# Performance work log

Hardware: AMD Instinct MI355X
Metric: run time of the kernel (lower is better)

Reference implementation:

```python
import jax, jax.numpy as jnp
import numpy as np

N_NODES = 20000
N_EDGES = 160000
N_GRAPHS = 64
X_DIM = 9
E_DIM = 1
U_RAW = 4096
U_DIM = 256
E_HID = 1024
E_OUT = 512
N_HID = 512
N_OUT = 1


def _lin_params(k, fan_in, fan_out):
    kw, kb = jax.random.split(k)
    bound = 1.0 / np.sqrt(fan_in)
    W = jax.random.uniform(kw, (fan_in, fan_out), jnp.float32, -bound, bound)
    b = jax.random.uniform(kb, (fan_out,), jnp.float32, -bound, bound)
    return W, b


def setup_inputs() -> dict:
    key = jax.random.key(0)
    ks = jax.random.split(key, 16)
    x = jax.random.normal(ks[0], (N_NODES, X_DIM), jnp.float32)
    edge_attr = jax.random.normal(ks[1], (N_EDGES, E_DIM), jnp.float32)
    u = jax.random.normal(ks[2], (N_GRAPHS, U_RAW), jnp.float32)
    edge_index = jax.random.randint(ks[3], (2, N_EDGES), 0, N_NODES, jnp.int64)
    batch = jax.random.randint(ks[4], (N_NODES,), 0, N_GRAPHS, jnp.int64)

    Wsel, bsel = _lin_params(ks[5], U_RAW, U_DIM)
    e_in = E_DIM + 2 * X_DIM + U_DIM  # 275
    eW1, eb1 = _lin_params(ks[6], e_in, E_HID)
    eW2, eb2 = _lin_params(ks[7], E_HID, E_HID)
    eW3, eb3 = _lin_params(ks[8], E_HID, E_HID)
    eW4, eb4 = _lin_params(ks[9], E_HID, E_HID)
    eW5, eb5 = _lin_params(ks[10], E_HID, E_OUT)
    n1W1, n1b1 = _lin_params(ks[11], E_OUT + X_DIM, N_HID)  # 521
    n1W2, n1b2 = _lin_params(ks[12], N_HID, N_HID)
    n2W1, n2b1 = _lin_params(ks[13], X_DIM + N_HID + U_DIM, N_HID)  # 777
    n2W2, n2b2 = _lin_params(ks[14], N_HID, N_OUT)

    return dict(x=x, edge_attr=edge_attr, u=u, edge_index=edge_index, batch=batch,
                Wsel=Wsel, bsel=bsel,
                eW1=eW1, eb1=eb1, eW2=eW2, eb2=eb2, eW3=eW3, eb3=eb3,
                eW4=eW4, eb4=eb4, eW5=eW5, eb5=eb5,
                n1W1=n1W1, n1b1=n1b1, n1W2=n1W2, n1b2=n1b2,
                n2W1=n2W1, n2b1=n2b1, n2W2=n2W2, n2b2=n2b2)


def _forward(x, edge_attr, u, edge_index, batch,
             Wsel, bsel, eW1, eb1, eW2, eb2, eW3, eb3, eW4, eb4, eW5, eb5,
             n1W1, n1b1, n1W2, n1b2, n2W1, n2b1, n2W2, n2b2):
    relu = jax.nn.relu
    u2 = u @ Wsel + bsel  # [B, 256]
    row, col = edge_index[0], edge_index[1]

    # EdgeModel: cat([src, dest, edge_attr, u[batch[row]]]) -> 5-layer MLP
    e = jnp.concatenate([x[row], x[col], edge_attr, u2[batch[row]]], axis=1)
    e = relu(e @ eW1 + eb1)
    e = relu(e @ eW2 + eb2)
    e = relu(e @ eW3 + eb3)
    e = relu(e @ eW4 + eb4)
    e = e @ eW5 + eb5  # [E, 512]

    # NodeModel: gather x[col], MLP1, scatter_mean over row, MLP2
    h = jnp.concatenate([x[col], e], axis=1)
    h = relu(h @ n1W1 + n1b1)
    h = relu(h @ n1W2 + n1b2)  # [E, 512]
    ssum = jax.ops.segment_sum(h, row, num_segments=x.shape[0])
    cnt = jax.ops.segment_sum(jnp.ones((h.shape[0],), h.dtype), row, num_segments=x.shape[0])
    agg = ssum / jnp.maximum(cnt, 1.0)[:, None]  # scatter_mean

    z = jnp.concatenate([x, agg, u2[batch]], axis=1)
    z = relu(z @ n2W1 + n2b1)
    z = z @ n2W2 + n2b2  # [N, 1]
    return jnp.squeeze(z)


def reference(x, edge_attr, u, edge_index, batch,
              Wsel, bsel, eW1, eb1, eW2, eb2, eW3, eb3, eW4, eb4, eW5, eb5,
              n1W1, n1b1, n1W2, n1b2, n2W1, n2b1, n2W2, n2b2):
    return _forward(x, edge_attr, u, edge_index, batch,
                    Wsel, bsel, eW1, eb1, eW2, eb2, eW3, eb3, eW4, eb4, eW5, eb5,
                    n1W1, n1b1, n1W2, n1b2, n2W1, n2b1, n2W2, n2b2)
```

## Files before the change

### kernel.cpp

```cpp
#include <hip/hip_runtime.h>

typedef _Float16 f16;
typedef __attribute__((ext_vector_type(8))) _Float16 f16x8;
typedef __attribute__((ext_vector_type(4))) float f32x4;

#define E_TOTAL 160000
#define NN 20000
#define NGRAPH 64

__device__ __forceinline__ void gl_lds16(const void* g, void* l) {
    __builtin_amdgcn_global_load_lds((const __attribute__((address_space(1))) void*)g,
                                     (__attribute__((address_space(3))) void*)l, 16, 0, 0);
}

#define MFMA16(a, b, c) __builtin_amdgcn_mfma_f32_16x16x32_f16((a), (b), (c), 0, 0, 0)
#define LGKM(n) do { asm volatile("s_waitcnt lgkmcnt(" #n ")" ::: "memory"); \
                     __builtin_amdgcn_sched_barrier(0); } while (0)
#define VMW4  asm volatile("s_waitcnt vmcnt(4)" ::: "memory")
#define VMW0  asm volatile("s_waitcnt vmcnt(0)" ::: "memory")
#define SBAR  __builtin_amdgcn_s_barrier()
#define SCHED0 __builtin_amdgcn_sched_barrier(0)

template <int RELU, int AUXU, int AUXX, int SCAT>
__global__ __launch_bounds__(512, 2) void hgemm8(
    int M, int N, int K,
    const f16* __restrict__ A, int lda,
    const f16* __restrict__ Bt,
    f16* __restrict__ C, int ldc,
    const float* __restrict__ bias,
    const f16* __restrict__ utab, const int* __restrict__ uidx,
    const float* __restrict__ x9, const int* __restrict__ xidx, const float* __restrict__ W9,
    float* __restrict__ sout, const int* __restrict__ sidx)
{
    __shared__ __align__(16) char Ash[2][2][16384];
    __shared__ __align__(16) char Bsh[2][2][16384];
    __shared__ float Ws9[AUXX ? 2304 : 1];

    const int tid  = threadIdx.x;
    const int lane = tid & 63;
    const int w    = tid >> 6;

    const int nbn = gridDim.x;
    const int nwg = nbn * gridDim.y;
    int d  = blockIdx.y * nbn + blockIdx.x;
    int q8 = nwg >> 3, r8 = nwg & 7;
    int xk = d & 7, j8 = d >> 3;
    int wl = (xk < r8 ? xk * (q8 + 1) : r8 * (q8 + 1) + (xk - r8) * q8) + j8;
    const int bm = (wl / nbn) * 256;
    const int bn = (wl % nbn) * 256;

    const int wm = (w >> 2) * 128;
    const int wn = (w & 3) * 64;
    const int fr = lane & 15;
    const int kq = lane >> 4;

    const char* Ab = (const char*)A;
    const char* Bb = (const char*)Bt;
    const size_t lda2 = (size_t)lda * 2;
    const size_t ldb2 = (size_t)K * 2;

    f32x4 acc[8][4] = {};

    int aoff[8], boff[4];
#pragma unroll
    for (int mi = 0; mi < 8; ++mi) {
        int r = wm + mi * 16 + fr;
        aoff[mi] = r * 64 + ((kq ^ ((r >> 1) & 3)) << 4);
    }
#pragma unroll
    for (int ni = 0; ni < 4; ++ni) {
        int r = wn + ni * 16 + fr;
        boff[ni] = r * 64 + ((kq ^ ((r >> 1) & 3)) << 4);
    }

    int sdest[2];
    size_t gsrcA[2], gsrcB[2];
#pragma unroll
    for (int i = 0; i < 2; ++i) {
        int L = i * 8192 + tid * 16;
        int row = L >> 6;
        int s = (L >> 4) & 3;
        int sw = (s ^ ((row >> 1) & 3)) << 4;
        sdest[i] = L;
        gsrcA[i] = (size_t)(bm + row) * lda2 + sw;
        gsrcB[i] = (size_t)(bn + row) * ldb2 + sw;
    }

    const int NT = K >> 6;

    auto stageA = [&](int t, int h, int buf) {
        size_t kb = (size_t)t * 128 + h * 64;
#pragma unroll
        for (int i = 0; i < 2; ++i)
            gl_lds16(Ab + gsrcA[i] + kb, &Ash[buf][h][0] + sdest[i]);
    };
    auto stageB = [&](int t, int h, int buf) {
        size_t kb = (size_t)t * 128 + h * 64;
#pragma unroll
        for (int i = 0; i < 2; ++i)
            gl_lds16(Bb + gsrcB[i] + kb, &Bsh[buf][h][0] + sdest[i]);
    };

    f16x8 a0[4], b0[4], a1[4], a2[4], b2[4], a3[4];

    stageA(0, 0, 0); stageB(0, 0, 0); stageA(0, 1, 0); stageB(0, 1, 0);
    VMW4;
    SBAR;
#pragma unroll
    for (int i = 0; i < 4; ++i) a0[i] = *(const f16x8*)(&Ash[0][0][0] + aoff[i]);
#pragma unroll
    for (int i = 0; i < 4; ++i) b0[i] = *(const f16x8*)(&Bsh[0][0][0] + boff[i]);

    for (int t = 0; t < NT; ++t) {
        const int cur = t & 1, nxt = cur ^ 1;
        const bool pre = (t + 1 < NT);
        const char* A0 = &Ash[cur][0][0];
        const char* A1 = &Ash[cur][1][0];
        const char* B1 = &Bsh[cur][1][0];

#pragma unroll
        for (int i = 0; i < 4; ++i) a1[i] = *(const f16x8*)(A0 + aoff[4 + i]);
        if (pre) stageA(t + 1, 0, nxt);
        SBAR;
        LGKM(4);
        __builtin_amdgcn_s_setprio(1);
#pragma unroll
        for (int mi = 0; mi < 4; ++mi)
#pragma unroll
            for (int ni = 0; ni < 4; ++ni)
                acc[mi][ni] = MFMA16(a0[mi], b0[ni], acc[mi][ni]);
        __builtin_amdgcn_s_setprio(0);
        SBAR;

        if (pre) stageB(t + 1, 0, nxt);
        SBAR;
        LGKM(0);
        if (pre) { VMW4; } else { VMW0; }
        SBAR;
#pragma unroll
        for (int i = 0; i < 4; ++i) a2[i] = *(const f16x8*)(A1 + aoff[i]);
#pragma unroll
        for (int i = 0; i < 4; ++i) b2[i] = *(const f16x8*)(B1 + boff[i]);
        SCHED0;
        __builtin_amdgcn_s_setprio(1);
#pragma unroll
        for (int mi = 0; mi < 4; ++mi)
#pragma unroll
            for (int ni = 0; ni < 4; ++ni)
                acc[4 + mi][ni] = MFMA16(a1[mi], b0[ni], acc[4 + mi][ni]);
        __builtin_amdgcn_s_setprio(0);
        SBAR;

#pragma unroll
        for (int i = 0; i < 4; ++i) a3[i] = *(const f16x8*)(A1 + aoff[4 + i]);
        if (pre) stageA(t + 1, 1, nxt);
        SBAR;
        LGKM(4);
        __builtin_amdgcn_s_setprio(1);
#pragma unroll
        for (int mi = 0; mi < 4; ++mi)
#pragma unroll
            for (int ni = 0; ni < 4; ++ni)
                acc[mi][ni] = MFMA16(a2[mi], b2[ni], acc[mi][ni]);
        __builtin_amdgcn_s_setprio(0);
        SBAR;

        if (pre) stageB(t + 1, 1, nxt);
        SBAR;
        LGKM(0);
        if (pre) {
            VMW4;
            SBAR;
            const char* An = &Ash[nxt][0][0];
            const char* Bn = &Bsh[nxt][0][0];
#pragma unroll
            for (int i = 0; i < 4; ++i) a0[i] = *(const f16x8*)(An + aoff[i]);
#pragma unroll
            for (int i = 0; i < 4; ++i) b0[i] = *(const f16x8*)(Bn + boff[i]);
            SCHED0;
        }
        __builtin_amdgcn_s_setprio(1);
#pragma unroll
        for (int mi = 0; mi < 4; ++mi)
#pragma unroll
            for (int ni = 0; ni < 4; ++ni)
                acc[4 + mi][ni] = MFMA16(a3[mi], b2[ni], acc[4 + mi][ni]);
        __builtin_amdgcn_s_setprio(0);
        SBAR;
    }

    if (AUXX) {
        for (int i = tid; i < 9 * 256; i += 512)
            Ws9[i] = W9[(size_t)(i >> 8) * N + bn + (i & 255)];
        __syncthreads();
    }

#pragma unroll
    for (int mi = 0; mi < 8; ++mi) {
        int r0 = bm + wm + mi * 16 + kq * 4;
#pragma unroll
        for (int r = 0; r < 4; ++r) {
            int grow = r0 + r;
            if (grow >= M) continue;
            int ub = 0;
            if (AUXU) ub = uidx[grow];
            int sb = 0;
            if (SCAT) sb = sidx[grow];
            float xv[9];
            if (AUXX) {
                int xi = xidx ? xidx[grow] : grow;
#pragma unroll
                for (int q = 0; q < 9; ++q) xv[q] = x9[(size_t)xi * 9 + q];
            }
#pragma unroll
            for (int ni = 0; ni < 4; ++ni) {
                int lcol = wn + ni * 16 + fr;
                int col = bn + lcol;
                float v = acc[mi][ni][r] + bias[col];
                if (AUXU) v += (float)utab[(size_t)ub * N + col];
                if (AUXX) {
                    float s = 0.f;
#pragma unroll
                    for (int q = 0; q < 9; ++q) s = fmaf(xv[q], Ws9[q * 256 + lcol], s);
                    v += s;
                }
                if (RELU) v = fmaxf(v, 0.f);
                if (SCAT) {
                    atomicAdd(sout + (size_t)sb * N + col, v);
                } else {
                    C[(size_t)grow * ldc + col] = (f16)v;
                }
            }
        }
    }
}

struct WtJob { const float* src; f16* dst; int r0, ks, n, kp, tr; };
struct WtJobs { WtJob j[10]; };

__global__ void k_wtall(WtJobs js)
{
    WtJob jb = js.j[blockIdx.y];
    size_t tot = (size_t)jb.n * jb.kp;
    size_t t = (size_t)blockIdx.x * 256 + threadIdx.x;
    if (t >= tot) return;
    if (jb.tr) {
        int n = (int)(t / jb.kp), k = (int)(t % jb.kp);
        jb.dst[t] = (k < jb.ks) ? (f16)jb.src[(size_t)(jb.r0 + k) * jb.n + n] : (f16)0.f;
    } else {
        jb.dst[t] = (f16)jb.src[t];
    }
}

__global__ void k_cbias(const float* __restrict__ n1W1, const float* __restrict__ eb5,
                        const float* __restrict__ n1b1, float* __restrict__ cb)
{
    int b = blockIdx.x * 256 + threadIdx.x;
    if (b >= 512) return;
    float s = n1b1[b];
    for (int c = 0; c < 512; ++c) s = fmaf(eb5[c], n1W1[(size_t)(9 + c) * 512 + b], s);
    cb[b] = s;
}

__global__ __launch_bounds__(256) void k_u2b(const float* __restrict__ u,
                                             const float* __restrict__ Wsel,
                                             const float* __restrict__ bsel,
                                             f16* __restrict__ u2h)
{
    __shared__ float us[4096];
    __shared__ float red[256];
    const int g = blockIdx.y;
    const int c0 = blockIdx.x * 16;
    const int col = threadIdx.x & 15;
    const int kp = threadIdx.x >> 4;
    for (int i = threadIdx.x; i < 4096; i += 256) us[i] = u[(size_t)g * 4096 + i];
    __syncthreads();
    float acc = 0.f;
    const float* wp = Wsel + (size_t)(kp * 256) * 256 + c0 + col;
#pragma unroll 8
    for (int i = 0; i < 256; ++i) acc = fmaf(us[kp * 256 + i], wp[(size_t)i * 256], acc);
    red[threadIdx.x] = acc;
    __syncthreads();
    if (kp < 8) red[threadIdx.x] += red[threadIdx.x + 128];
    __syncthreads();
    if (kp < 4) red[threadIdx.x] += red[threadIdx.x + 64];
    __syncthreads();
    if (kp < 2) red[threadIdx.x] += red[threadIdx.x + 32];
    __syncthreads();
    if (kp == 0)
        u2h[(size_t)g * 256 + c0 + col] = (f16)(red[threadIdx.x] + red[threadIdx.x + 16] + bsel[c0 + col]);
}

__global__ void k_gather19(const float* __restrict__ x, const float* __restrict__ eattr,
                           const int* __restrict__ ei, const int* __restrict__ batch,
                           f16* __restrict__ feat, int* __restrict__ ebat)
{
    size_t t = (size_t)blockIdx.x * 256 + threadIdx.x;
    if (t >= (size_t)E_TOTAL * 64) return;
    int i = (int)(t >> 6), j = (int)(t & 63);
    float v = 0.f;
    if (j < 9)        v = x[ei[i] * 9 + j];
    else if (j < 18)  v = x[ei[E_TOTAL + i] * 9 + (j - 9)];
    else if (j == 18) v = eattr[i];
    else if (j == 19) ebat[i] = batch[ei[i]];
    feat[t] = (f16)v;
}

__global__ void k_cnt(const int* __restrict__ ei, float* __restrict__ cnt)
{
    int t = blockIdx.x * 256 + threadIdx.x;
    if (t < E_TOTAL) atomicAdd(cnt + ei[t], 1.0f);
}

__global__ void k_agg(const float* __restrict__ ssum, const float* __restrict__ cnt,
                      f16* __restrict__ agg)
{
    size_t t = (size_t)blockIdx.x * 256 + threadIdx.x;
    if (t >= (size_t)NN * 512) return;
    int n = (int)(t >> 9);
    agg[t] = (f16)(ssum[t] / fmaxf(cnt[n], 1.f));
}

__global__ void k_final(const f16* __restrict__ z1, const float* __restrict__ W,
                        const float* __restrict__ b, float* __restrict__ out)
{
    int gt = blockIdx.x * 256 + threadIdx.x;
    int row = gt >> 6;
    int lane = threadIdx.x & 63;
    if (row >= NN) return;
    float s = 0.f;
#pragma unroll
    for (int c = lane; c < 512; c += 64) s += (float)z1[(size_t)row * 512 + c] * W[c];
#pragma unroll
    for (int off = 32; off; off >>= 1) s += __shfl_down(s, off);
    if (lane == 0) out[row] = s + b[0];
}


extern "C" void kernel_launch(void* const* d_in, const int* in_sizes, int n_in,
                              void* d_out, int out_size, void* d_ws, size_t ws_size,
                              hipStream_t stream)
{
    const float* x     = (const float*)d_in[0];
    const float* eattr = (const float*)d_in[1];
    const float* u     = (const float*)d_in[2];
    const int*   ei    = (const int*)d_in[3];
    const int*   batch = (const int*)d_in[4];
    const float* Wsel  = (const float*)d_in[5];
    const float* bsel  = (const float*)d_in[6];
    const float* eW1 = (const float*)d_in[7],  * eb1 = (const float*)d_in[8];
    const float* eW2 = (const float*)d_in[9],  * eb2 = (const float*)d_in[10];
    const float* eW3 = (const float*)d_in[11], * eb3 = (const float*)d_in[12];
    const float* eW4 = (const float*)d_in[13], * eb4 = (const float*)d_in[14];
    const float* eW5 = (const float*)d_in[15], * eb5 = (const float*)d_in[16];
    const float* n1W1 = (const float*)d_in[17], * n1b1 = (const float*)d_in[18];
    const float* n1W2 = (const float*)d_in[19], * n1b2 = (const float*)d_in[20];
    const float* n2W1 = (const float*)d_in[21], * n2b1 = (const float*)d_in[22];
    const float* n2W2 = (const float*)d_in[23], * n2b2 = (const float*)d_in[24];
    float* out = (float*)d_out;

    char* ws = (char*)d_ws;
    size_t off = 0;
    auto alc = [&](size_t bytes) { char* p = ws + off; off += (bytes + 255) & ~(size_t)255; return p; };

    float* ssum  = (float*)alc((size_t)NN * 512 * 4);
    float* cnt   = (float*)alc((size_t)NN * 4);
    float* zbias = (float*)alc(1024 * 4);
    float* cbias = (float*)alc(512 * 4);
    f16* u2h     = (f16*)alc((size_t)256 * 256 * 2);
    f16* ubias_e = (f16*)alc((size_t)64 * 1024 * 2);
    f16* ubias_n = (f16*)alc((size_t)64 * 512 * 2);
    f16* eW1t19  = (f16*)alc((size_t)1024 * 64 * 2);
    f16* eW1ut   = (f16*)alc((size_t)1024 * 256 * 2);
    f16* eW2t    = (f16*)alc((size_t)1024 * 1024 * 2);
    f16* eW3t    = (f16*)alc((size_t)1024 * 1024 * 2);
    f16* eW4t    = (f16*)alc((size_t)1024 * 1024 * 2);
    f16* eW5h    = (f16*)alc((size_t)1024 * 512 * 2);
    f16* combo_t = (f16*)alc((size_t)512 * 1024 * 2);
    f16* n1W1et  = (f16*)alc((size_t)512 * 512 * 2);
    f16* n1W2t   = (f16*)alc((size_t)512 * 512 * 2);
    f16* n2W1et  = (f16*)alc((size_t)512 * 512 * 2);
    f16* n2W1ut  = (f16*)alc((size_t)512 * 256 * 2);
    f16* featAll = (f16*)alc((size_t)E_TOTAL * 64 * 2);
    int* ebatAll = (int*)alc((size_t)E_TOTAL * 4);
    size_t fixed = off;

    size_t per_edge = 4096;
    size_t need_ro = (size_t)20224 * 512 * 2 * 2;
    size_t avail = ws_size > fixed ? ws_size - fixed : 0;
    long long Cmax = (long long)(avail / per_edge);
    int C;
    if (Cmax >= E_TOTAL)      C = E_TOTAL;
    else if (Cmax >= 16384)   C = (int)((Cmax / 16384) * 16384);
    else                      C = (int)((Cmax / 256) * 256);
    if ((size_t)C * per_edge < need_ro)
        C = (int)(((need_ro + per_edge - 1) / per_edge + 255) / 256 * 256);

    f16* buf1 = (f16*)(ws + fixed);
    f16* buf2 = buf1 + (size_t)C * 1024;
    f16* agg  = (f16*)(ws + fixed);
    f16* z1   = agg + (size_t)20224 * 512;

    size_t zlen = (size_t)((char*)cbias - (char*)ssum) + 512 * 4;
    hipMemsetAsync(ssum, 0, zlen, stream);

    WtJobs js;
    js.j[0] = {eW1,  eW1t19, 0,   19,   1024, 64,   1};
    js.j[1] = {eW1,  eW1ut,  19,  256,  1024, 256,  1};
    js.j[2] = {eW2,  eW2t,   0,   1024, 1024, 1024, 1};
    js.j[3] = {eW3,  eW3t,   0,   1024, 1024, 1024, 1};
    js.j[4] = {eW4,  eW4t,   0,   1024, 1024, 1024, 1};
    js.j[5] = {n1W1, n1W1et, 9,   512,  512,  512,  1};
    js.j[6] = {n1W2, n1W2t,  0,   512,  512,  512,  1};
    js.j[7] = {n2W1, n2W1et, 9,   512,  512,  512,  1};
    js.j[8] = {n2W1, n2W1ut, 521, 256,  512,  256,  1};
    js.j[9] = {eW5,  eW5h,   0,   0,    1024, 512,  0};
    k_wtall<<<dim3(4096, 10), 256, 0, stream>>>(js);

    k_u2b<<<dim3(16, NGRAPH), 256, 0, stream>>>(u, Wsel, bsel, u2h);
    k_cnt<<<(E_TOTAL + 255) / 256, 256, 0, stream>>>(ei, cnt);
    k_cbias<<<2, 256, 0, stream>>>(n1W1, eb5, n1b1, cbias);
    k_gather19<<<(unsigned)(((size_t)E_TOTAL * 64 + 255) / 256), 256, 0, stream>>>(
        x, eattr, ei, batch, featAll, ebatAll);

    hgemm8<0,0,0,0><<<dim3(4, 1), 512, 0, stream>>>(64, 1024, 256, u2h, 256, eW1ut,
        ubias_e, 1024, eb1, nullptr, nullptr, nullptr, nullptr, nullptr, nullptr, nullptr);
    hgemm8<0,0,0,0><<<dim3(2, 1), 512, 0, stream>>>(64, 512, 256, u2h, 256, n2W1ut,
        ubias_n, 512, n2b1, nullptr, nullptr, nullptr, nullptr, nullptr, nullptr, nullptr);

    hgemm8<0,0,0,0><<<dim3(4, 2), 512, 0, stream>>>(512, 1024, 512, n1W1et, 512, eW5h,
        combo_t, 1024, zbias, nullptr, nullptr, nullptr, nullptr, nullptr, nullptr, nullptr);

    for (int e0 = 0; e0 < E_TOTAL; e0 += C) {
        int Ce = E_TOTAL - e0 < C ? E_TOTAL - e0 : C;
        int gy = (Ce + 255) / 256;

        hgemm8<1,1,0,0><<<dim3(4, gy), 512, 0, stream>>>(Ce, 1024, 64,
            featAll + (size_t)e0 * 64, 64, eW1t19,
            buf1, 1024, zbias, ubias_e, ebatAll + e0, nullptr, nullptr, nullptr, nullptr, nullptr);
        hgemm8<1,0,0,0><<<dim3(4, gy), 512, 0, stream>>>(Ce, 1024, 1024, buf1, 1024, eW2t,
            buf2, 1024, eb2, nullptr, nullptr, nullptr, nullptr, nullptr, nullptr, nullptr);
        hgemm8<1,0,0,0><<<dim3(4, gy), 512, 0, stream>>>(Ce, 1024, 1024, buf2, 1024, eW3t,
            buf1, 1024, eb3, nullptr, nullptr, nullptr, nullptr, nullptr, nullptr, nullptr);
        hgemm8<1,0,0,0><<<dim3(4, gy), 512, 0, stream>>>(Ce, 1024, 1024, buf1, 1024, eW4t,
            buf2, 1024, eb4, nullptr, nullptr, nullptr, nullptr, nullptr, nullptr, nullptr);

        hgemm8<1,0,1,0><<<dim3(2, gy), 512, 0, stream>>>(Ce, 512, 1024, buf2, 1024, combo_t,
            buf1, 512, cbias, nullptr, nullptr, x, ei + E_TOTAL + e0, n1W1, nullptr, nullptr);

        hgemm8<1,0,0,1><<<dim3(2, gy), 512, 0, stream>>>(Ce, 512, 512, buf1, 512, n1W2t,
            nullptr, 512, n1b2, nullptr, nullptr, nullptr, nullptr, nullptr, ssum, ei + e0);
    }

    k_agg<<<(unsigned)(((size_t)NN * 512 + 255) / 256), 256, 0, stream>>>(ssum, cnt, agg);
    hgemm8<1,1,1,0><<<dim3(2, 79), 512, 0, stream>>>(NN, 512, 512, agg, 512, n2W1et,
        z1, 512, zbias, ubias_n, batch, x, nullptr, n2W1, nullptr, nullptr);
    k_final<<<(NN * 64 + 255) / 256, 256, 0, stream>>>(z1, n2W2, n2b2, out);
}
```

Baseline: 2.213 ms.

## Add 256x512-tile triple-buffered GEMM for the three 1024x1024 edge layers

```diff
diff --git a/kernel.cpp b/kernel.cpp
--- a/kernel.cpp
+++ b/kernel.cpp
@@ -16,10 +16,124 @@
 #define MFMA16(a, b, c) __builtin_amdgcn_mfma_f32_16x16x32_f16((a), (b), (c), 0, 0, 0)
 #define LGKM(n) do { asm volatile("s_waitcnt lgkmcnt(" #n ")" ::: "memory"); \
                      __builtin_amdgcn_sched_barrier(0); } while (0)
+#define VMW6  asm volatile("s_waitcnt vmcnt(6)" ::: "memory")
 #define VMW4  asm volatile("s_waitcnt vmcnt(4)" ::: "memory")
 #define VMW0  asm volatile("s_waitcnt vmcnt(0)" ::: "memory")
 #define SBAR  __builtin_amdgcn_s_barrier()
 #define SCHED0 __builtin_amdgcn_sched_barrier(0)
+
+__global__ __launch_bounds__(512) void hgemmW(
+    int M, int N, int K,
+    const f16* __restrict__ A, int lda,
+    const f16* __restrict__ Bt,
+    f16* __restrict__ C, int ldc,
+    const float* __restrict__ bias)
+{
+    __shared__ __align__(16) char L[3][49152];
+    const int tid  = threadIdx.x;
+    const int lane = tid & 63;
+    const int w    = tid >> 6;
+
+    const int nbn = gridDim.x;
+    const int nwg = nbn * gridDim.y;
+    int d  = blockIdx.y * nbn + blockIdx.x;
+    int q8 = nwg >> 3, r8 = nwg & 7;
+    int xk = d & 7, j8 = d >> 3;
+    int wl = (xk < r8 ? xk * (q8 + 1) : r8 * (q8 + 1) + (xk - r8) * q8) + j8;
+    const int bm = (wl / nbn) * 256;
+    const int bn = (wl % nbn) * 512;
+
+    const int wm = (w >> 2) * 128;
+    const int wn = (w & 3) * 128;
+    const int fr = lane & 15;
+    const int kq = lane >> 4;
+
+    const char* Ab = (const char*)A;
+    const char* Bb = (const char*)Bt;
+    const size_t lda2 = (size_t)lda * 2;
+    const size_t ldb2 = (size_t)K * 2;
+
+    f32x4 acc[8][8] = {};
+
+    int aoff[8], boff[8];
+#pragma unroll
+    for (int mi = 0; mi < 8; ++mi) {
+        int r = wm + mi * 16 + fr;
+        aoff[mi] = r * 64 + ((kq ^ ((r >> 1) & 3)) << 4);
+    }
+#pragma unroll
+    for (int ni = 0; ni < 8; ++ni) {
+        int r = wn + ni * 16 + fr;
+        boff[ni] = 16384 + r * 64 + ((kq ^ ((r >> 1) & 3)) << 4);
+    }
+
+    int sdest[6];
+    size_t gsrcA[2], gsrcB[4];
+#pragma unroll
+    for (int i = 0; i < 6; ++i) {
+        int Lo = i * 8192 + tid * 16;
+        int row = Lo >> 6;
+        int slot = (Lo >> 4) & 3;
+        int sw = (slot ^ ((row >> 1) & 3)) << 4;
+        sdest[i] = Lo;
+        if (i < 2) gsrcA[i] = (size_t)(bm + row) * lda2 + sw;
+        else       gsrcB[i - 2] = (size_t)(bn + row - 256) * ldb2 + sw;
+    }
+
+    auto stage = [&](int t, int buf) {
+        size_t kb = (size_t)t * 64;
+#pragma unroll
+        for (int i = 0; i < 2; ++i) gl_lds16(Ab + gsrcA[i] + kb, &L[buf][0] + sdest[i]);
+#pragma unroll
+        for (int i = 0; i < 4; ++i) gl_lds16(Bb + gsrcB[i] + kb, &L[buf][0] + sdest[2 + i]);
+    };
+
+    const int NT = K >> 5;
+    stage(0, 0);
+    stage(1, 1);
+
+    int buf = 0;
+    for (int t = 0; t < NT; ++t) {
+        if (t + 1 < NT) { VMW6; } else { VMW0; }
+        SBAR;
+        const char* base = &L[buf][0];
+        f16x8 a[8], b[8];
+#pragma unroll
+        for (int i = 0; i < 8; ++i) a[i] = *(const f16x8*)(base + aoff[i]);
+#pragma unroll
+        for (int i = 0; i < 8; ++i) b[i] = *(const f16x8*)(base + boff[i]);
+        int nb = buf + 2; if (nb >= 3) nb -= 3;
+        if (t + 2 < NT) stage(t + 2, nb);
+        LGKM(0);
+        __builtin_amdgcn_s_setprio(1);
+#pragma unroll
+        for (int mi = 0; mi < 8; ++mi)
+#pragma unroll
+            for (int ni = 0; ni < 8; ++ni)
+                acc[mi][ni] = MFMA16(a[mi], b[ni], acc[mi][ni]);
+        __builtin_amdgcn_s_setprio(0);
+        ++buf; if (buf == 3) buf = 0;
+    }
+
+    float bz[8];
+#pragma unroll
+    for (int ni = 0; ni < 8; ++ni) bz[ni] = bias[bn + wn + ni * 16 + fr];
+#pragma unroll
+    for (int mi = 0; mi < 8; ++mi) {
+        int r0 = bm + wm + mi * 16 + kq * 4;
+#pragma unroll
+        for (int r = 0; r < 4; ++r) {
+            int grow = r0 + r;
+            if (grow >= M) continue;
+#pragma unroll
+            for (int ni = 0; ni < 8; ++ni) {
+                int col = bn + wn + ni * 16 + fr;
+                float v = fmaxf(acc[mi][ni][r] + bz[ni], 0.f);
+                C[(size_t)grow * ldc + col] = (f16)v;
+            }
+        }
+    }
+}
 
 template <int RELU, int AUXU, int AUXX, int SCAT>
 __global__ __launch_bounds__(512, 2) void hgemm8(
@@ -77,11 +191,11 @@
     size_t gsrcA[2], gsrcB[2];
 #pragma unroll
     for (int i = 0; i < 2; ++i) {
-        int L = i * 8192 + tid * 16;
-        int row = L >> 6;
-        int s = (L >> 4) & 3;
+        int Lo = i * 8192 + tid * 16;
+        int row = Lo >> 6;
+        int s = (Lo >> 4) & 3;
         int sw = (s ^ ((row >> 1) & 3)) << 4;
-        sdest[i] = L;
+        sdest[i] = Lo;
         gsrcA[i] = (size_t)(bm + row) * lda2 + sw;
         gsrcB[i] = (size_t)(bn + row) * ldb2 + sw;
     }
@@ -438,12 +552,10 @@
         hgemm8<1,1,0,0><<<dim3(4, gy), 512, 0, stream>>>(Ce, 1024, 64,
             featAll + (size_t)e0 * 64, 64, eW1t19,
             buf1, 1024, zbias, ubias_e, ebatAll + e0, nullptr, nullptr, nullptr, nullptr, nullptr);
-        hgemm8<1,0,0,0><<<dim3(4, gy), 512, 0, stream>>>(Ce, 1024, 1024, buf1, 1024, eW2t,
-            buf2, 1024, eb2, nullptr, nullptr, nullptr, nullptr, nullptr, nullptr, nullptr);
-        hgemm8<1,0,0,0><<<dim3(4, gy), 512, 0, stream>>>(Ce, 1024, 1024, buf2, 1024, eW3t,
-            buf1, 1024, eb3, nullptr, nullptr, nullptr, nullptr, nullptr, nullptr, nullptr);
-        hgemm8<1,0,0,0><<<dim3(4, gy), 512, 0, stream>>>(Ce, 1024, 1024, buf1, 1024, eW4t,
-            buf2, 1024, eb4, nullptr, nullptr, nullptr, nullptr, nullptr, nullptr, nullptr);
+
+        hgemmW<<<dim3(2, gy), 512, 0, stream>>>(Ce, 1024, 1024, buf1, 1024, eW2t, buf2, 1024, eb2);
+        hgemmW<<<dim3(2, gy), 512, 0, stream>>>(Ce, 1024, 1024, buf2, 1024, eW3t, buf1, 1024, eb3);
+        hgemmW<<<dim3(2, gy), 512, 0, stream>>>(Ce, 1024, 1024, buf1, 1024, eW4t, buf2, 1024, eb4);
 
         hgemm8<1,0,1,0><<<dim3(2, gy), 512, 0, stream>>>(Ce, 512, 1024, buf2, 1024, combo_t,
             buf1, 512, cbias, nullptr, nullptr, x, ei + E_TOTAL + e0, n1W1, nullptr, nullptr);
```

Measured after the change: 8.306 ms. 275% more time.

## Load B operand straight from global into registers, bypassing LDS

Applied to the files above, without the earlier changes.

```diff
diff --git a/kernel.cpp b/kernel.cpp
--- a/kernel.cpp
+++ b/kernel.cpp
@@ -16,13 +16,15 @@
 #define MFMA16(a, b, c) __builtin_amdgcn_mfma_f32_16x16x32_f16((a), (b), (c), 0, 0, 0)
 #define LGKM(n) do { asm volatile("s_waitcnt lgkmcnt(" #n ")" ::: "memory"); \
                      __builtin_amdgcn_sched_barrier(0); } while (0)
-#define VMW4  asm volatile("s_waitcnt vmcnt(4)" ::: "memory")
+#define VMW12 asm volatile("s_waitcnt vmcnt(12)" ::: "memory")
 #define VMW0  asm volatile("s_waitcnt vmcnt(0)" ::: "memory")
 #define SBAR  __builtin_amdgcn_s_barrier()
 #define SCHED0 __builtin_amdgcn_sched_barrier(0)
 
+struct BF { f16x8 v[4][2]; };
+
 template <int RELU, int AUXU, int AUXX, int SCAT>
-__global__ __launch_bounds__(512, 2) void hgemm8(
+__global__ __launch_bounds__(512, 2) void hgemmB(
     int M, int N, int K,
     const f16* __restrict__ A, int lda,
     const f16* __restrict__ Bt,
@@ -33,7 +35,6 @@
     float* __restrict__ sout, const int* __restrict__ sidx)
 {
     __shared__ __align__(16) char Ash[2][2][16384];
-    __shared__ __align__(16) char Bsh[2][2][16384];
     __shared__ float Ws9[AUXX ? 2304 : 1];
 
     const int tid  = threadIdx.x;
@@ -61,133 +62,89 @@
 
     f32x4 acc[8][4] = {};
 
-    int aoff[8], boff[4];
+    int aoff[8];
 #pragma unroll
     for (int mi = 0; mi < 8; ++mi) {
         int r = wm + mi * 16 + fr;
         aoff[mi] = r * 64 + ((kq ^ ((r >> 1) & 3)) << 4);
     }
-#pragma unroll
-    for (int ni = 0; ni < 4; ++ni) {
-        int r = wn + ni * 16 + fr;
-        boff[ni] = r * 64 + ((kq ^ ((r >> 1) & 3)) << 4);
-    }
 
     int sdest[2];
-    size_t gsrcA[2], gsrcB[2];
+    size_t gsrcA[2];
 #pragma unroll
     for (int i = 0; i < 2; ++i) {
-        int L = i * 8192 + tid * 16;
-        int row = L >> 6;
-        int s = (L >> 4) & 3;
+        int Lo = i * 8192 + tid * 16;
+        int row = Lo >> 6;
+        int s = (Lo >> 4) & 3;
         int sw = (s ^ ((row >> 1) & 3)) << 4;
-        sdest[i] = L;
+        sdest[i] = Lo;
         gsrcA[i] = (size_t)(bm + row) * lda2 + sw;
-        gsrcB[i] = (size_t)(bn + row) * ldb2 + sw;
-    }
+    }
+
+    const char* bbase[4];
+#pragma unroll
+    for (int ni = 0; ni < 4; ++ni)
+        bbase[ni] = Bb + (size_t)(bn + wn + ni * 16 + fr) * ldb2 + kq * 16;
 
     const int NT = K >> 6;
 
-    auto stageA = [&](int t, int h, int buf) {
-        size_t kb = (size_t)t * 128 + h * 64;
-#pragma unroll
-        for (int i = 0; i < 2; ++i)
-            gl_lds16(Ab + gsrcA[i] + kb, &Ash[buf][h][0] + sdest[i]);
+    auto stageA = [&](int t, int buf) {
+        size_t kb = (size_t)t << 7;
+#pragma unroll
+        for (int h = 0; h < 2; ++h)
+#pragma unroll
+            for (int i = 0; i < 2; ++i)
+                gl_lds16(Ab + gsrcA[i] + kb + h * 64, &Ash[buf][h][0] + sdest[i]);
     };
-    auto stageB = [&](int t, int h, int buf) {
-        size_t kb = (size_t)t * 128 + h * 64;
-#pragma unroll
-        for (int i = 0; i < 2; ++i)
-            gl_lds16(Bb + gsrcB[i] + kb, &Bsh[buf][h][0] + sdest[i]);
+    auto loadB = [&](BF& dst, int t) {
+        size_t kb = (size_t)t << 7;
+#pragma unroll
+        for (int ni = 0; ni < 4; ++ni)
+#pragma unroll
+            for (int ks = 0; ks < 2; ++ks)
+                dst.v[ni][ks] = *(const f16x8*)(bbase[ni] + kb + ks * 64);
     };
-
-    f16x8 a0[4], b0[4], a1[4], a2[4], b2[4], a3[4];
-
-    stageA(0, 0, 0); stageB(0, 0, 0); stageA(0, 1, 0); stageB(0, 1, 0);
-    VMW4;
-    SBAR;
-#pragma unroll
-    for (int i = 0; i < 4; ++i) a0[i] = *(const f16x8*)(&Ash[0][0][0] + aoff[i]);
-#pragma unroll
-    for (int i = 0; i < 4; ++i) b0[i] = *(const f16x8*)(&Bsh[0][0][0] + boff[i]);
-
-    for (int t = 0; t < NT; ++t) {
-        const int cur = t & 1, nxt = cur ^ 1;
+    auto body = [&](int t, int buf, const BF& cur, BF& nxt) {
         const bool pre = (t + 1 < NT);
-        const char* A0 = &Ash[cur][0][0];
-        const char* A1 = &Ash[cur][1][0];
-        const char* B1 = &Bsh[cur][1][0];
-
-#pragma unroll
-        for (int i = 0; i < 4; ++i) a1[i] = *(const f16x8*)(A0 + aoff[4 + i]);
-        if (pre) stageA(t + 1, 0, nxt);
+        if (pre) {
+            stageA(t + 1, buf ^ 1);
+            loadB(nxt, t + 1);
+            SCHED0;
+            VMW12;
+        } else {
+            VMW0;
+        }
         SBAR;
-        LGKM(4);
-        __builtin_amdgcn_s_setprio(1);
-#pragma unroll
-        for (int mi = 0; mi < 4; ++mi)
-#pragma unroll
-            for (int ni = 0; ni < 4; ++ni)
-                acc[mi][ni] = MFMA16(a0[mi], b0[ni], acc[mi][ni]);
-        __builtin_amdgcn_s_setprio(0);
+#pragma unroll
+        for (int ks = 0; ks < 2; ++ks) {
+            const char* half = &Ash[buf][ks][0];
+#pragma unroll
+            for (int g = 0; g < 2; ++g) {
+                f16x8 a[4];
+#pragma unroll
+                for (int i = 0; i < 4; ++i) a[i] = *(const f16x8*)(half + aoff[g * 4 + i]);
+                LGKM(0);
+                __builtin_amdgcn_s_setprio(1);
+#pragma unroll
+                for (int mi = 0; mi < 4; ++mi)
+#pragma unroll
+                    for (int ni = 0; ni < 4; ++ni)
+                        acc[g * 4 + mi][ni] = MFMA16(a[mi], cur.v[ni][ks], acc[g * 4 + mi][ni]);
+                __builtin_amdgcn_s_setprio(0);
+            }
+        }
         SBAR;
-
-        if (pre) stageB(t + 1, 0, nxt);
-        SBAR;
-        LGKM(0);
-        if (pre) { VMW4; } else { VMW0; }
-        SBAR;
-#pragma unroll
-        for (int i = 0; i < 4; ++i) a2[i] = *(const f16x8*)(A1 + aoff[i]);
-#pragma unroll
-        for (int i = 0; i < 4; ++i) b2[i] = *(const f16x8*)(B1 + boff[i]);
-        SCHED0;
-        __builtin_amdgcn_s_setprio(1);
-#pragma unroll
-        for (int mi = 0; mi < 4; ++mi)
-#pragma unroll
-            for (int ni = 0; ni < 4; ++ni)
-                acc[4 + mi][ni] = MFMA16(a1[mi], b0[ni], acc[4 + mi][ni]);
-        __builtin_amdgcn_s_setprio(0);
-        SBAR;
-
-#pragma unroll
-        for (int i = 0; i < 4; ++i) a3[i] = *(const f16x8*)(A1 + aoff[4 + i]);
-        if (pre) stageA(t + 1, 1, nxt);
-        SBAR;
-        LGKM(4);
-        __builtin_amdgcn_s_setprio(1);
-#pragma unroll
-        for (int mi = 0; mi < 4; ++mi)
-#pragma unroll
-            for (int ni = 0; ni < 4; ++ni)
-                acc[mi][ni] = MFMA16(a2[mi], b2[ni], acc[mi][ni]);
-        __builtin_amdgcn_s_setprio(0);
-        SBAR;
-
-        if (pre) stageB(t + 1, 1, nxt);
-        SBAR;
-        LGKM(0);
-        if (pre) {
-            VMW4;
-            SBAR;
-            const char* An = &Ash[nxt][0][0];
-            const char* Bn = &Bsh[nxt][0][0];
-#pragma unroll
-            for (int i = 0; i < 4; ++i) a0[i] = *(const f16x8*)(An + aoff[i]);
-#pragma unroll
-            for (int i = 0; i < 4; ++i) b0[i] = *(const f16x8*)(Bn + boff[i]);
-            SCHED0;
-        }
-        __builtin_amdgcn_s_setprio(1);
-#pragma unroll
-        for (int mi = 0; mi < 4; ++mi)
-#pragma unroll
-            for (int ni = 0; ni < 4; ++ni)
-                acc[4 + mi][ni] = MFMA16(a3[mi], b2[ni], acc[4 + mi][ni]);
-        __builtin_amdgcn_s_setprio(0);
-        SBAR;
-    }
+    };
+
+    BF bf0, bf1;
+    stageA(0, 0);
+    loadB(bf0, 0);
+    int t = 0;
+    for (; t + 2 <= NT; t += 2) {
+        body(t,     0, bf0, bf1);
+        body(t + 1, 1, bf1, bf0);
+    }
+    if (t < NT) body(t, t & 1, bf0, bf1);
 
     if (AUXX) {
         for (int i = tid; i < 9 * 256; i += 512)
@@ -423,37 +380,37 @@
     k_gather19<<<(unsigned)(((size_t)E_TOTAL * 64 + 255) / 256), 256, 0, stream>>>(
         x, eattr, ei, batch, featAll, ebatAll);
 
-    hgemm8<0,0,0,0><<<dim3(4, 1), 512, 0, stream>>>(64, 1024, 256, u2h, 256, eW1ut,
+    hgemmB<0,0,0,0><<<dim3(4, 1), 512, 0, stream>>>(64, 1024, 256, u2h, 256, eW1ut,
         ubias_e, 1024, eb1, nullptr, nullptr, nullptr, nullptr, nullptr, nullptr, nullptr);
-    hgemm8<0,0,0,0><<<dim3(2, 1), 512, 0, stream>>>(64, 512, 256, u2h, 256, n2W1ut,
+    hgemmB<0,0,0,0><<<dim3(2, 1), 512, 0, stream>>>(64, 512, 256, u2h, 256, n2W1ut,
         ubias_n, 512, n2b1, nullptr, nullptr, nullptr, nullptr, nullptr, nullptr, nullptr);
 
-    hgemm8<0,0,0,0><<<dim3(4, 2), 512, 0, stream>>>(512, 1024, 512, n1W1et, 512, eW5h,
+    hgemmB<0,0,0,0><<<dim3(4, 2), 512, 0, stream>>>(512, 1024, 512, n1W1et, 512, eW5h,
         combo_t, 1024, zbias, nullptr, nullptr, nullptr, nullptr, nullptr, nullptr, nullptr);
 
     for (int e0 = 0; e0 < E_TOTAL; e0 += C) {
         int Ce = E_TOTAL - e0 < C ? E_TOTAL - e0 : C;
         int gy = (Ce + 255) / 256;
 
-        hgemm8<1,1,0,0><<<dim3(4, gy), 512, 0, stream>>>(Ce, 1024, 64,
+        hgemmB<1,1,0,0><<<dim3(4, gy), 512, 0, stream>>>(Ce, 1024, 64,
             featAll + (size_t)e0 * 64, 64, eW1t19,
             buf1, 1024, zbias, ubias_e, ebatAll + e0, nullptr, nullptr, nullptr, nullptr, nullptr);
-        hgemm8<1,0,0,0><<<dim3(4, gy), 512, 0, stream>>>(Ce, 1024, 1024, buf1, 1024, eW2t,
+        hgemmB<1,0,0,0><<<dim3(4, gy), 512, 0, stream>>>(Ce, 1024, 1024, buf1, 1024, eW2t,
             buf2, 1024, eb2, nullptr, nullptr, nullptr, nullptr, nullptr, nullptr, nullptr);
-        hgemm8<1,0,0,0><<<dim3(4, gy), 512, 0, stream>>>(Ce, 1024, 1024, buf2, 1024, eW3t,
+        hgemmB<1,0,0,0><<<dim3(4, gy), 512, 0, stream>>>(Ce, 1024, 1024, buf2, 1024, eW3t,
             buf1, 1024, eb3, nullptr, nullptr, nullptr, nullptr, nullptr, nullptr, nullptr);
-        hgemm8<1,0,0,0><<<dim3(4, gy), 512, 0, stream>>>(Ce, 1024, 1024, buf1, 1024, eW4t,
+        hgemmB<1,0,0,0><<<dim3(4, gy), 512, 0, stream>>>(Ce, 1024, 1024, buf1, 1024, eW4t,
             buf2, 1024, eb4, nullptr, nullptr, nullptr, nullptr, nullptr, nullptr, nullptr);
 
-        hgemm8<1,0,1,0><<<dim3(2, gy), 512, 0, stream>>>(Ce, 512, 1024, buf2, 1024, combo_t,
+        hgemmB<1,0,1,0><<<dim3(2, gy), 512, 0, stream>>>(Ce, 512, 1024, buf2, 1024, combo_t,
             buf1, 512, cbias, nullptr, nullptr, x, ei + E_TOTAL + e0, n1W1, nullptr, nullptr);
 
-        hgemm8<1,0,0,1><<<dim3(2, gy), 512, 0, stream>>>(Ce, 512, 512, buf1, 512, n1W2t,
+        hgemmB<1,0,0,1><<<dim3(2, gy), 512, 0, stream>>>(Ce, 512, 512, buf1, 512, n1W2t,
             nullptr, 512, n1b2, nullptr, nullptr, nullptr, nullptr, nullptr, ssum, ei + e0);
     }
 
     k_agg<<<(unsigned)(((size_t)NN * 512 + 255) / 256), 256, 0, stream>>>(ssum, cnt, agg);
-    hgemm8<1,1,1,0><<<dim3(2, 79), 512, 0, stream>>>(NN, 512, 512, agg, 512, n2W1et,
+    hgemmB<1,1,1,0><<<dim3(2, 79), 512, 0, stream>>>(NN, 512, 512, agg, 512, n2W1et,
         z1, 512, zbias, ubias_n, batch, x, nullptr, n2W1, nullptr, nullptr);
     k_final<<<(NN * 64 + 255) / 256, 256, 0, stream>>>(z1, n2W2, n2b2, out);
 }
```

Measured after the change: 4.088 ms. 84.7% more time.

## Sort edges by source node and replace atomic scatter with segmented reduction

Applied to the files above, without the earlier changes.

```diff
diff --git a/kernel.cpp b/kernel.cpp
--- a/kernel.cpp
+++ b/kernel.cpp
@@ -21,7 +21,7 @@
 #define SBAR  __builtin_amdgcn_s_barrier()
 #define SCHED0 __builtin_amdgcn_sched_barrier(0)
 
-template <int RELU, int AUXU, int AUXX, int SCAT>
+template <int RELU, int AUXU, int AUXX>
 __global__ __launch_bounds__(512, 2) void hgemm8(
     int M, int N, int K,
     const f16* __restrict__ A, int lda,
@@ -29,8 +29,7 @@
     f16* __restrict__ C, int ldc,
     const float* __restrict__ bias,
     const f16* __restrict__ utab, const int* __restrict__ uidx,
-    const float* __restrict__ x9, const int* __restrict__ xidx, const float* __restrict__ W9,
-    float* __restrict__ sout, const int* __restrict__ sidx)
+    const float* __restrict__ x9, const int* __restrict__ xidx, const float* __restrict__ W9)
 {
     __shared__ __align__(16) char Ash[2][2][16384];
     __shared__ __align__(16) char Bsh[2][2][16384];
@@ -77,11 +76,11 @@
     size_t gsrcA[2], gsrcB[2];
 #pragma unroll
     for (int i = 0; i < 2; ++i) {
-        int L = i * 8192 + tid * 16;
-        int row = L >> 6;
-        int s = (L >> 4) & 3;
+        int Lo = i * 8192 + tid * 16;
+        int row = Lo >> 6;
+        int s = (Lo >> 4) & 3;
         int sw = (s ^ ((row >> 1) & 3)) << 4;
-        sdest[i] = L;
+        sdest[i] = Lo;
         gsrcA[i] = (size_t)(bm + row) * lda2 + sw;
         gsrcB[i] = (size_t)(bn + row) * ldb2 + sw;
     }
@@ -204,8 +203,6 @@
             if (grow >= M) continue;
             int ub = 0;
             if (AUXU) ub = uidx[grow];
-            int sb = 0;
-            if (SCAT) sb = sidx[grow];
             float xv[9];
             if (AUXX) {
                 int xi = xidx ? xidx[grow] : grow;
@@ -225,11 +222,7 @@
                     v += s;
                 }
                 if (RELU) v = fmaxf(v, 0.f);
-                if (SCAT) {
-                    atomicAdd(sout + (size_t)sb * N + col, v);
-                } else {
-                    C[(size_t)grow * ldc + col] = (f16)v;
-                }
+                C[(size_t)grow * ldc + col] = (f16)v;
             }
         }
     }
@@ -291,25 +284,86 @@
         u2h[(size_t)g * 256 + c0 + col] = (f16)(red[threadIdx.x] + red[threadIdx.x + 16] + bsel[c0 + col]);
 }
 
+__global__ void k_cnt(const int* __restrict__ ei, float* __restrict__ cnt)
+{
+    int t = blockIdx.x * 256 + threadIdx.x;
+    if (t < E_TOTAL) atomicAdd(cnt + ei[t], 1.0f);
+}
+
+__global__ __launch_bounds__(256) void k_scan(const float* __restrict__ cnt,
+                                              int* __restrict__ offs, int* __restrict__ cursor)
+{
+    __shared__ int part[256];
+    const int tid = threadIdx.x;
+    const int n0 = tid * 79;
+    int s = 0;
+    for (int i = 0; i < 79; ++i) {
+        int n = n0 + i;
+        if (n < NN) s += (int)cnt[n];
+    }
+    part[tid] = s;
+    __syncthreads();
+    for (int dstep = 1; dstep < 256; dstep <<= 1) {
+        int add = (tid >= dstep) ? part[tid - dstep] : 0;
+        __syncthreads();
+        part[tid] += add;
+        __syncthreads();
+    }
+    int run = part[tid] - s;
+    for (int i = 0; i < 79; ++i) {
+        int n = n0 + i;
+        if (n < NN) {
+            offs[n] = run;
+            cursor[n] = run;
+            run += (int)cnt[n];
+        }
+    }
+    if (tid == 255) offs[NN] = E_TOTAL;
+}
+
+__global__ void k_perm(const int* __restrict__ ei, int* __restrict__ cursor,
+                       int* __restrict__ perm)
+{
+    int e = blockIdx.x * 256 + threadIdx.x;
+    if (e < E_TOTAL) {
+        int pos = atomicAdd(cursor + ei[e], 1);
+        perm[pos] = e;
+    }
+}
+
 __global__ void k_gather19(const float* __restrict__ x, const float* __restrict__ eattr,
                            const int* __restrict__ ei, const int* __restrict__ batch,
-                           f16* __restrict__ feat, int* __restrict__ ebat)
+                           const int* __restrict__ perm,
+                           f16* __restrict__ feat, int* __restrict__ ebat, int* __restrict__ colA)
 {
     size_t t = (size_t)blockIdx.x * 256 + threadIdx.x;
     if (t >= (size_t)E_TOTAL * 64) return;
-    int i = (int)(t >> 6), j = (int)(t & 63);
+    int j = (int)(t >> 6), jj = (int)(t & 63);
+    int e = perm[j];
     float v = 0.f;
-    if (j < 9)        v = x[ei[i] * 9 + j];
-    else if (j < 18)  v = x[ei[E_TOTAL + i] * 9 + (j - 9)];
-    else if (j == 18) v = eattr[i];
-    else if (j == 19) ebat[i] = batch[ei[i]];
+    if (jj < 9)        v = x[ei[e] * 9 + jj];
+    else if (jj < 18)  v = x[ei[E_TOTAL + e] * 9 + (jj - 9)];
+    else if (jj == 18) v = eattr[e];
+    else if (jj == 19) ebat[j] = batch[ei[e]];
+    else if (jj == 20) colA[j] = ei[E_TOTAL + e];
     feat[t] = (f16)v;
 }
 
-__global__ void k_cnt(const int* __restrict__ ei, float* __restrict__ cnt)
-{
-    int t = blockIdx.x * 256 + threadIdx.x;
-    if (t < E_TOTAL) atomicAdd(cnt + ei[t], 1.0f);
+__global__ void k_seg(int e0, int Ce, const f16* __restrict__ h2,
+                      const int* __restrict__ offs, float* __restrict__ ssum)
+{
+    size_t t = (size_t)blockIdx.x * 256 + threadIdx.x;
+    if (t >= (size_t)NN * 512) return;
+    int n = (int)(t >> 9), col = (int)(t & 511);
+    int lo = offs[n], hi = offs[n + 1];
+    int e1 = e0 + Ce;
+    if (lo < e0) lo = e0;
+    if (hi > e1) hi = e1;
+    if (lo >= hi) return;
+    float s = 0.f;
+    for (int j = lo; j < hi; ++j)
+        s += (float)h2[(size_t)(j - e0) * 512 + col];
+    ssum[t] += s;
 }
 
 __global__ void k_agg(const float* __restrict__ ssum, const float* __restrict__ cnt,
@@ -381,8 +435,12 @@
     f16* n1W2t   = (f16*)alc((size_t)512 * 512 * 2);
     f16* n2W1et  = (f16*)alc((size_t)512 * 512 * 2);
     f16* n2W1ut  = (f16*)alc((size_t)512 * 256 * 2);
+    int* offs    = (int*)alc((size_t)(NN + 1) * 4);
+    int* cursor  = (int*)alc((size_t)NN * 4);
+    int* perm    = (int*)alc((size_t)E_TOTAL * 4);
     f16* featAll = (f16*)alc((size_t)E_TOTAL * 64 * 2);
     int* ebatAll = (int*)alc((size_t)E_TOTAL * 4);
+    int* colAll  = (int*)alc((size_t)E_TOTAL * 4);
     size_t fixed = off;
 
     size_t per_edge = 4096;
@@ -419,41 +477,46 @@
 
     k_u2b<<<dim3(16, NGRAPH), 256, 0, stream>>>(u, Wsel, bsel, u2h);
     k_cnt<<<(E_TOTAL + 255) / 256, 256, 0, stream>>>(ei, cnt);
+    k_scan<<<1, 256, 0, stream>>>(cnt, offs, cursor);
+    k_perm<<<(E_TOTAL + 255) / 256, 256, 0, stream>>>(ei, cursor, perm);
     k_cbias<<<2, 256, 0, stream>>>(n1W1, eb5, n1b1, cbias);
     k_gather19<<<(unsigned)(((size_t)E_TOTAL * 64 + 255) / 256), 256, 0, stream>>>(
-        x, eattr, ei, batch, featAll, ebatAll);
-
-    hgemm8<0,0,0,0><<<dim3(4, 1), 512, 0, stream>>>(64, 1024, 256, u2h, 256, eW1ut,
-        ubias_e, 1024, eb1, nullptr, nullptr, nullptr, nullptr, nullptr, nullptr, nullptr);
-    hgemm8<0,0,0,0><<<dim3(2, 1), 512, 0, stream>>>(64, 512, 256, u2h, 256, n2W1ut,
-        ubias_n, 512, n2b1, nullptr, nullptr, nullptr, nullptr, nullptr, nullptr, nullptr);
-
-    hgemm8<0,0,0,0><<<dim3(4, 2), 512, 0, stream>>>(512, 1024, 512, n1W1et, 512, eW5h,
-        combo_t, 1024, zbias, nullptr, nullptr, nullptr, nullptr, nullptr, nullptr, nullptr);
+        x, eattr, ei, batch, perm, featAll, ebatAll, colAll);
+
+    hgemm8<0,0,0><<<dim3(4, 1), 512, 0, stream>>>(64, 1024, 256, u2h, 256, eW1ut,
+        ubias_e, 1024, eb1, nullptr, nullptr, nullptr, nullptr, nullptr);
+    hgemm8<0,0,0><<<dim3(2, 1), 512, 0, stream>>>(64, 512, 256, u2h, 256, n2W1ut,
+        ubias_n, 512, n2b1, nullptr, nullptr, nullptr, nullptr, nullptr);
+
+    hgemm8<0,0,0><<<dim3(4, 2), 512, 0, stream>>>(512, 1024, 512, n1W1et, 512, eW5h,
+        combo_t, 1024, zbias, nullptr, nullptr, nullptr, nullptr, nullptr);
 
     for (int e0 = 0; e0 < E_TOTAL; e0 += C) {
         int Ce = E_TOTAL - e0 < C ? E_TOTAL - e0 : C;
         int gy = (Ce + 255) / 256;
 
-        hgemm8<1,1,0,0><<<dim3(4, gy), 512, 0, stream>>>(Ce, 1024, 64,
+        hgemm8<1,1,0><<<dim3(4, gy), 512, 0, stream>>>(Ce, 1024, 64,
             featAll + (size_t)e0 * 64, 64, eW1t19,
-            buf1, 1024, zbias, ubias_e, ebatAll + e0, nullptr, nullptr, nullptr, nullptr, nullptr);
-        hgemm8<1,0,0,0><<<dim3(4, gy), 512, 0, stream>>>(Ce, 1024, 1024, buf1, 1024, eW2t,
-            buf2, 1024, eb2, nullptr, nullptr, nullptr, nullptr, nullptr, nullptr, nullptr);
-        hgemm8<1,0,0,0><<<dim3(4, gy), 512, 0, stream>>>(Ce, 1024, 1024, buf2, 1024, eW3t,
-            buf1, 1024, eb3, nullptr, nullptr, nullptr, nullptr, nullptr, nullptr, nullptr);
-        hgemm8<1,0,0,0><<<dim3(4, gy), 512, 0, stream>>>(Ce, 1024, 1024, buf1, 1024, eW4t,
-            buf2, 1024, eb4, nullptr, nullptr, nullptr, nullptr, nullptr, nullptr, nullptr);
-
-        hgemm8<1,0,1,0><<<dim3(2, gy), 512, 0, stream>>>(Ce, 512, 1024, buf2, 1024, combo_t,
-            buf1, 512, cbias, nullptr, nullptr, x, ei + E_TOTAL + e0, n1W1, nullptr, nullptr);
-
-        hgemm8<1,0,0,1><<<dim3(2, gy), 512, 0, stream>>>(Ce, 512, 512, buf1, 512, n1W2t,
-            nullptr, 512, n1b2, nullptr, nullptr, nullptr, nullptr, nullptr, ssum, ei + e0);
+            buf1, 1024, zbias, ubias_e, ebatAll + e0, nullptr, nullptr, nullptr);
+        hgemm8<1,0,0><<<dim3(4, gy), 512, 0, stream>>>(Ce, 1024, 1024, buf1, 1024, eW2t,
+            buf2, 1024, eb2, nullptr, nullptr, nullptr, nullptr, nullptr);
+        hgemm8<1,0,0><<<dim3(4, gy), 512, 0, stream>>>(Ce, 1024, 1024, buf2, 1024, eW3t,
+            buf1, 1024, eb3, nullptr, nullptr, nullptr, nullptr, nullptr);
+        hgemm8<1,0,0><<<dim3(4, gy), 512, 0, stream>>>(Ce, 1024, 1024, buf1, 1024, eW4t,
+            buf2, 1024, eb4, nullptr, nullptr, nullptr, nullptr, nullptr);
+
+        hgemm8<1,0,1><<<dim3(2, gy), 512, 0, stream>>>(Ce, 512, 1024, buf2, 1024, combo_t,
+            buf1, 512, cbias, nullptr, nullptr, x, colAll + e0, n1W1);
+
+        hgemm8<1,0,0><<<dim3(2, gy), 512, 0, stream>>>(Ce, 512, 512, buf1, 512, n1W2t,
+            buf2, 512, n1b2, nullptr, nullptr, nullptr, nullptr, nullptr);
+
+        k_seg<<<(unsigned)(((size_t)NN * 512 + 255) / 256), 256, 0, stream>>>(
+            e0, Ce, buf2, offs, ssum);
     }
 
     k_agg<<<(unsigned)(((size_t)NN * 512 + 255) / 256), 256, 0, stream>>>(ssum, cnt, agg);
-    hgemm8<1,1,1,0><<<dim3(2, 79), 512, 0, stream>>>(NN, 512, 512, agg, 512, n2W1et,
-        z1, 512, zbias, ubias_n, batch, x, nullptr, n2W1, nullptr, nullptr);
+    hgemm8<1,1,1><<<dim3(2, 79), 512, 0, stream>>>(NN, 512, 512, agg, 512, n2W1et,
+        z1, 512, zbias, ubias_n, batch, x, nullptr, n2W1);
     k_final<<<(NN * 64 + 255) / 256, 256, 0, stream>>>(z1, n2W2, n2b2, out);
 }
```

Result: no change. 2.171 ms (-1.9%).
